# Kernel optimization log

Hardware: AMD Instinct MI355X
Metric: run time of the kernel (lower is better)

The kernel has to match this reference:

```python
import jax, jax.numpy as jnp
import numpy as np

ANCHORS = np.array([[10,13],[16,30],[33,23],[30,61],[62,45],[59,119],[116,90],[156,198],[373,326]], dtype=np.float32)
STRIDES = [32, 16, 8]
MASKS = [[6,7,8],[3,4,5],[0,1,2]]
N_CLASSES = 80
IGNORE_THRESH = 0.7
NUM_A = 3


def _bce_logits(x, z):
    # binary_cross_entropy_with_logits, elementwise (reduction applied by caller)
    return jnp.maximum(x, 0.0) - x * z + jnp.log1p(jnp.exp(-jnp.abs(x)))


def _layer_loss(output, labels, stride, anch_mask):
    B, C, H, W = output.shape
    n_ch = 5 + N_CLASSES
    dtype = output.dtype
    ref_wh = jnp.asarray(ANCHORS / stride, dtype)              # (9,2) all anchors in grid units
    m_anch = ref_wh[jnp.asarray(anch_mask)]                    # (3,2) anchors for this layer
    group = anch_mask[0] // 3                                   # which triple of ref anchors matches this layer

    # (B, A, H, W, n_ch) raw logits
    out = output.reshape(B, NUM_A, n_ch, H, W).transpose(0, 1, 3, 4, 2)

    # decoded pred boxes (cx, cy, w, h) in grid units
    xs = jnp.arange(W, dtype=dtype)
    ys = jnp.arange(H, dtype=dtype)
    px = jax.nn.sigmoid(out[..., 0]) + xs[None, None, None, :]
    py = jax.nn.sigmoid(out[..., 1]) + ys[None, None, :, None]
    pw = jnp.exp(out[..., 2]) * m_anch[:, 0][None, :, None, None]
    ph = jnp.exp(out[..., 3]) * m_anch[:, 1][None, :, None, None]
    pred = jnp.stack([px, py, pw, ph], axis=-1)                # (B,A,H,W,4)

    NC = NUM_A * H * W

    def build_one(pred_b, lab):
        # lab: (nL, 5) = [class, x, y, w, h] normalized; all rows assumed valid
        tx = lab[:, 1] * W; ty = lab[:, 2] * H
        tw = lab[:, 3] * W; th = lab[:, 4] * H
        ti = tx.astype(jnp.int32); tj = ty.astype(jnp.int32)
        wh = jnp.stack([tw, th], axis=-1)                      # (nL,2)

        # anchor IoU (boxes anchored at origin) against all 9 ref anchors
        mn = jnp.minimum(wh[:, None, :], ref_wh[None, :, :])
        en = jnp.prod((mn > 0).astype(dtype), axis=-1)
        inter = jnp.prod(mn, axis=-1) * en
        a_iou = inter / (jnp.prod(wh, -1)[:, None] + jnp.prod(ref_wh, -1)[None, :] - inter)
        best_all = jnp.argmax(a_iou, axis=1)                   # (nL,)
        best_n = best_all % 3
        matched = (best_all // 3) == group                     # truth belongs to this layer

        # pairwise IoU pred boxes vs truth boxes (cxcywh)
        tb = jnp.stack([tx, ty, tw, th], axis=-1)              # (nL,4)
        pf = pred_b.reshape(-1, 4)                             # (AHW,4)
        tl = jnp.maximum(pf[:, None, :2] - pf[:, None, 2:] / 2, tb[None, :, :2] - tb[None, :, 2:] / 2)
        br = jnp.minimum(pf[:, None, :2] + pf[:, None, 2:] / 2, tb[None, :, :2] + tb[None, :, 2:] / 2)
        en2 = jnp.prod((tl < br).astype(dtype), axis=-1)
        inter2 = jnp.prod(br - tl, axis=-1) * en2
        pious = inter2 / (jnp.prod(pf[:, 2:], -1)[:, None] + jnp.prod(tb[:, 2:], -1)[None, :] - inter2)
        obj = (jnp.max(pious, axis=1) <= IGNORE_THRESH).astype(dtype)  # (AHW,) = ~ignore

        # scatter matched truths into (a, j, i) cells; unmatched go to dummy slot NC
        lin = jnp.where(matched, (best_n * H + tj) * W + ti, NC)
        obj = jnp.concatenate([obj, jnp.zeros((1,), dtype)]).at[lin].set(1.0)[:NC].reshape(NUM_A, H, W)
        sel = jnp.zeros((NC + 1,), dtype).at[lin].set(1.0)[:NC].reshape(NUM_A, H, W)
        sval = jnp.sqrt(2.0 - tw * th / (H * W))
        scale = jnp.zeros((NC + 1,), dtype).at[lin].set(sval)[:NC].reshape(NUM_A, H, W)

        cls = lab[:, 0].astype(jnp.int32)
        rows = jnp.concatenate([
            (tx - ti.astype(dtype))[:, None],
            (ty - tj.astype(dtype))[:, None],
            jnp.log(tw / m_anch[best_n, 0] + 1e-16)[:, None],
            jnp.log(th / m_anch[best_n, 1] + 1e-16)[:, None],
            jnp.ones((lab.shape[0], 1), dtype),
            jax.nn.one_hot(cls, N_CLASSES, dtype=dtype)], axis=-1)      # (nL, n_ch)
        target = jnp.zeros((NC + 1, n_ch), dtype).at[lin].set(rows)[:NC].reshape(NUM_A, H, W, n_ch)
        return target, obj, sel, scale

    target, obj, sel, scale = jax.vmap(build_one)(pred, labels)

    sel_e = sel[..., None]
    sc_e = scale[..., None]
    oxy = out[..., :2] * sel_e;              txy = target[..., :2] * sel_e
    owh = out[..., 2:4] * sel_e * sc_e;      twh = target[..., 2:4] * sel_e * sc_e
    o4 = out[..., 4] * obj;                  t4 = target[..., 4] * obj
    ocl = out[..., 5:] * sel_e;              tcl = target[..., 5:] * sel_e

    loss_xy = jnp.sum(_bce_logits(oxy, txy) * sc_e * sc_e)
    loss_wh = jnp.sum((owh - twh) ** 2) / 2
    loss_obj = jnp.sum(_bce_logits(o4, t4))
    loss_cls = jnp.sum(_bce_logits(ocl, tcl))
    return loss_xy + loss_wh + loss_obj + loss_cls


def setup_inputs() -> dict:
    key = jax.random.key(0)
    k0, k1, k2, kc, kxy, kwh = jax.random.split(key, 6)
    B, nL = 16, 50
    output0 = jax.random.normal(k0, (B, 255, 19, 19), dtype=jnp.float32)
    output1 = jax.random.normal(k1, (B, 255, 38, 38), dtype=jnp.float32)
    output2 = jax.random.normal(k2, (B, 255, 76, 76), dtype=jnp.float32)
    cls = jax.random.randint(kc, (B, nL, 1), 0, N_CLASSES).astype(jnp.float32)
    xy = jax.random.uniform(kxy, (B, nL, 2), minval=0.05, maxval=0.95)
    wh = jax.random.uniform(kwh, (B, nL, 2), minval=0.05, maxval=0.4)
    targets = jnp.concatenate([cls, xy, wh], axis=-1)  # [class, x, y, w, h], all rows valid
    return {"output0": output0, "output1": output1, "output2": output2, "targets": targets}


def reference(output0, output1, output2, targets):
    outs = [output0, output1, output2]
    loss = jnp.float32(0.0)
    for layer_no, o in enumerate(outs):
        loss = loss + _layer_loss(o, targets, STRIDES[layer_no], MASKS[layer_no])
    return loss
```

## Files before the change

kernel.cpp:

```cpp
#include <hip/hip_runtime.h>
#include <math.h>

#define N_LABELS 50
#define NCLS 80
#define LOG2C 0.693147180559945f
#define N_CORR_BLOCKS 12
#define N_MAIN_BLOCKS 736
#define N_BLOCKS (N_MAIN_BLOCKS + N_CORR_BLOCKS)

__device__ __constant__ float d_anchors[9][2] = {
    {10.f,13.f},{16.f,30.f},{33.f,23.f},{30.f,61.f},{62.f,45.f},
    {59.f,119.f},{116.f,90.f},{156.f,198.f},{373.f,326.f}
};

__device__ float g_slots[64];
__device__ int   g_count;

__device__ __forceinline__ float softplus_f(float x) {
    return fmaxf(x, 0.f) + __logf(1.f + __expf(-fabsf(x)));
}
__device__ __forceinline__ float bce_f(float x, float z) {
    return fmaxf(x, 0.f) - x * z + __logf(1.f + __expf(-fabsf(x)));
}
__device__ __forceinline__ float sigmoid_f(float x) {
    return __builtin_amdgcn_rcpf(1.f + __expf(-x));
}

template<int H, int W, int GROUP>
__device__ __forceinline__ float main_part(const float* __restrict__ out,
        const float* __restrict__ tgt, int b, int chunk,
        float4* sbox, float* sta)
{
    constexpr int HW = H * W;
    constexpr int NC = 3 * HW;
    constexpr int STRIDE = 608 / W;
    int tid = threadIdx.x;

    if (tid < N_LABELS) {
        const float* lp = tgt + ((size_t)b * N_LABELS + tid) * 5;
        float tx = lp[1] * (float)W, ty = lp[2] * (float)H;
        float tw = lp[3] * (float)W, th = lp[4] * (float)H;
        sbox[tid] = make_float4(tx - 0.5f*tw, ty - 0.5f*th, tx + 0.5f*tw, ty + 0.5f*th);
        sta[tid] = tw * th * (0.7f / 1.7f);
    }
    __syncthreads();

    const float* ob = out + (size_t)b * 255 * HW;
    int c0i = chunk * 512 + tid;
    float x0[2], x1[2], y0[2], y1[2], p07[2], c4v[2], whb[2];
    bool valid[2], ign[2];

    #pragma unroll
    for (int k = 0; k < 2; ++k) {
        int cell = c0i + k * 256;
        valid[k] = (cell < NC);
        int cc = valid[k] ? cell : 0;
        int a = cc / HW, rem = cc - a * HW;
        int hh = rem / W, ww = rem - hh * W;
        const float* base = ob + (size_t)a * 85 * HW + rem;
        float c0 = base[0];
        float c1 = base[HW];
        float c2 = base[2 * (size_t)HW];
        float c3 = base[3 * (size_t)HW];
        c4v[k] = base[4 * (size_t)HW];
        float aw = d_anchors[GROUP*3 + a][0] * (1.f / (float)STRIDE);
        float ah = d_anchors[GROUP*3 + a][1] * (1.f / (float)STRIDE);
        float pw = __expf(c2) * aw, ph = __expf(c3) * ah;
        float px = sigmoid_f(c0) + (float)ww;
        float py = sigmoid_f(c1) + (float)hh;
        x0[k] = px - 0.5f*pw; x1[k] = px + 0.5f*pw;
        y0[k] = py - 0.5f*ph; y1[k] = py + 0.5f*ph;
        p07[k] = pw * ph * (0.7f / 1.7f);
        whb[k] = 0.5f * (c2*c2 + c3*c3);
        ign[k] = false;
    }

    #pragma unroll 5
    for (int l = 0; l < N_LABELS; ++l) {
        float4 tb = sbox[l];
        float ta07 = sta[l];
        #pragma unroll
        for (int k = 0; k < 2; ++k) {
            float w_ = fminf(x1[k], tb.z) - fmaxf(x0[k], tb.x);
            float h_ = fminf(y1[k], tb.w) - fmaxf(y0[k], tb.y);
            bool hit = (fminf(w_, h_) > 0.f) && (w_ * h_ > ta07 + p07[k]);
            ign[k] = ign[k] || hit;
        }
    }

    float lsum = 0.f;
    #pragma unroll
    for (int k = 0; k < 2; ++k)
        if (valid[k])
            lsum += (ign[k] ? LOG2C : softplus_f(c4v[k])) + 80.f * LOG2C + whb[k];
    return lsum;
}

template<int H, int W, int STRIDE, int GROUP>
__device__ __forceinline__ float corr_part(const float* __restrict__ out,
        const float* __restrict__ tgt, int bbase,
        float4 (*sbox)[N_LABELS], int* slin)
{
    constexpr int HW = H * W;
    int tid = threadIdx.x, wid = tid >> 6, lane = tid & 63;
    int b = bbase + wid;

    float tx=0, ty=0, tw=0, th=0, lw=0, lh=0, sc=0;
    int lin = -1, cls = 0;
    if (lane < N_LABELS) {
        const float* lp = tgt + ((size_t)b * N_LABELS + lane) * 5;
        cls = (int)lp[0];
        tx = lp[1] * (float)W; ty = lp[2] * (float)H;
        tw = lp[3] * (float)W; th = lp[4] * (float)H;
        float ta = tw * th;
        sbox[wid][lane] = make_float4(tx - 0.5f*tw, ty - 0.5f*th, tx + 0.5f*tw, ty + 0.5f*th);
        float best_iou = -1.f; int best = 0;
        #pragma unroll
        for (int kk = 0; kk < 9; ++kk) {
            float rw = d_anchors[kk][0] * (1.f / (float)STRIDE);
            float rh = d_anchors[kk][1] * (1.f / (float)STRIDE);
            float mx = fminf(tw, rw), my = fminf(th, rh);
            float inter = (mx > 0.f && my > 0.f) ? mx * my : 0.f;
            float iou = inter / (ta + rw * rh - inter);
            if (iou > best_iou) { best_iou = iou; best = kk; }
        }
        int bn = best - (best / 3) * 3;
        float aw = d_anchors[GROUP*3 + bn][0] * (1.f / (float)STRIDE);
        float ah = d_anchors[GROUP*3 + bn][1] * (1.f / (float)STRIDE);
        lw = __logf(tw / aw + 1e-16f);
        lh = __logf(th / ah + 1e-16f);
        sc = sqrtf(2.f - tw * th * (1.f / (float)HW));
        if (best / 3 == GROUP) {
            int ti = (int)tx, tj = (int)ty;
            lin = (bn * H + tj) * W + ti;
        }
    }
    slin[wid * 64 + lane] = lin;
    __syncthreads();

    bool active = (lin >= 0);
    if (active) {
        for (int l2 = lane + 1; l2 < N_LABELS; ++l2)
            if (slin[wid * 64 + l2] == lin) active = false;
    }

    float lsum = 0.f;
    if (active) {
        int a = lin / HW, rem = lin - a * HW;
        int hh = rem / W, ww = rem - hh * W;
        const float* base = out + ((size_t)b * 255 + (size_t)a * 85) * HW + rem;
        float c0 = base[0];
        float c1 = base[HW];
        float c2 = base[2 * (size_t)HW];
        float c3 = base[3 * (size_t)HW];
        float c4 = base[4 * (size_t)HW];
        float aw = d_anchors[GROUP*3 + a][0] * (1.f / (float)STRIDE);
        float ah = d_anchors[GROUP*3 + a][1] * (1.f / (float)STRIDE);
        float pw = __expf(c2) * aw, ph = __expf(c3) * ah;
        float px = sigmoid_f(c0) + (float)ww;
        float py = sigmoid_f(c1) + (float)hh;
        float X0 = px - 0.5f*pw, X1 = px + 0.5f*pw;
        float Y0 = py - 0.5f*ph, Y1 = py + 0.5f*ph;
        float p07 = pw * ph * (0.7f / 1.7f);
        bool ign = false;
        for (int l = 0; l < N_LABELS; ++l) {
            float4 tb = sbox[wid][l];
            float ta07 = (tb.z - tb.x) * (tb.w - tb.y) * (0.7f / 1.7f);
            float w_ = fminf(X1, tb.z) - fmaxf(X0, tb.x);
            float h_ = fminf(Y1, tb.w) - fmaxf(Y0, tb.y);
            ign = ign || ((fminf(w_, h_) > 0.f) && (w_ * h_ > ta07 + p07));
        }
        float baseobj = ign ? LOG2C : softplus_f(c4);
        lsum += bce_f(c4, 1.f) - baseobj;
        float s2 = sc * sc;
        float txf = tx - (float)(int)tx, tyf = ty - (float)(int)ty;
        lsum += (bce_f(c0, txf) + bce_f(c1, tyf)) * s2;
        float dw = c2 - lw, dh = c3 - lh;
        lsum += 0.5f * (dw*dw + dh*dh) * s2;
        float csum = 0.f;
        for (int c = 0; c < NCLS; ++c) {
            float lg = base[(size_t)(5 + c) * HW];
            csum += bce_f(lg, (c == cls) ? 1.f : 0.f);
        }
        lsum += csum - 80.f * LOG2C;
    }
    return lsum;
}

__global__ __launch_bounds__(256) void yolo_main(
        const float* __restrict__ o0, const float* __restrict__ o1,
        const float* __restrict__ o2, const float* __restrict__ tgt,
        float* __restrict__ loss)
{
    __shared__ float4 sbox[4][N_LABELS];
    __shared__ float  sta4[4][N_LABELS];
    __shared__ int    slin[4 * 64];
    __shared__ float  wsums[4];
    __shared__ int    sflag;
    int bid = blockIdx.x, tid = threadIdx.x;

    float lsum;
    if (bid < N_CORR_BLOCKS) {
        int layer = bid >> 2, bbase = (bid & 3) * 4;
        if (layer == 0)      lsum = corr_part<19,19,32,2>(o0, tgt, bbase, sbox, slin);
        else if (layer == 1) lsum = corr_part<38,38,16,1>(o1, tgt, bbase, sbox, slin);
        else                 lsum = corr_part<76,76,8,0>(o2, tgt, bbase, sbox, slin);
    } else {
        int mb = bid - N_CORR_BLOCKS;
        if (mb < 48) {
            lsum = main_part<19,19,2>(o0, tgt, mb / 3, mb % 3, &sbox[0][0], &sta4[0][0]);
        } else if (mb < 192) {
            int id = mb - 48;
            lsum = main_part<38,38,1>(o1, tgt, id / 9, id % 9, &sbox[0][0], &sta4[0][0]);
        } else {
            int id = mb - 192;
            lsum = main_part<76,76,0>(o2, tgt, id / 34, id % 34, &sbox[0][0], &sta4[0][0]);
        }
    }

    #pragma unroll
    for (int off = 32; off > 0; off >>= 1)
        lsum += __shfl_down(lsum, off);
    if ((tid & 63) == 0) wsums[tid >> 6] = lsum;
    __syncthreads();

    if (tid == 0) {
        float tot = wsums[0] + wsums[1] + wsums[2] + wsums[3];
        float old = atomicAdd(&g_slots[bid & 63], tot);
        asm volatile("" :: "v"(old) : "memory");
        int cnt = atomicAdd(&g_count, 1);
        sflag = (cnt == N_BLOCKS - 1) ? 1 : 0;
    }
    __syncthreads();

    if (sflag && tid < 64) {
        float v = __hip_atomic_load(&g_slots[tid], __ATOMIC_RELAXED, __HIP_MEMORY_SCOPE_AGENT);
        #pragma unroll
        for (int off = 32; off > 0; off >>= 1)
            v += __shfl_down(v, off);
        __hip_atomic_store(&g_slots[tid], 0.f, __ATOMIC_RELAXED, __HIP_MEMORY_SCOPE_AGENT);
        if (tid == 0) {
            *loss = v;
            __hip_atomic_store(&g_count, 0, __ATOMIC_RELAXED, __HIP_MEMORY_SCOPE_AGENT);
        }
    }
}

extern "C" void kernel_launch(void* const* d_in, const int* in_sizes, int n_in,
                              void* d_out, int out_size, void* d_ws, size_t ws_size,
                              hipStream_t stream) {
    const float* o0  = (const float*)d_in[0];
    const float* o1  = (const float*)d_in[1];
    const float* o2  = (const float*)d_in[2];
    const float* tgt = (const float*)d_in[3];
    float* loss = (float*)d_out;
    yolo_main<<<N_BLOCKS, 256, 0, stream>>>(o0, o1, o2, tgt, loss);
}
```

Measured before the change: 27.77 us.

## Spread completion counters across padded slots and branchless ignore test

Replaces the single global completion counter with 64 per-slot counters padded to separate cache lines, plus a second-level done counter, so the 748 blocks no longer all contend on one atomic. Each slot's last arriver bumps the done counter, and the final one reduces the slots. Separately, the IoU ignore test is rewritten as a running max of a min-combined margin using fma, avoiding boolean logic in the inner label loop. This adds a two-level atomic protocol, and the ignore decision may differ slightly at boundary cases because of the fma rounding.

```diff
diff --git a/kernel.cpp b/kernel.cpp
--- a/kernel.cpp
+++ b/kernel.cpp
@@ -13,8 +13,9 @@
     {59.f,119.f},{116.f,90.f},{156.f,198.f},{373.f,326.f}
 };
 
-__device__ float g_slots[64];
-__device__ int   g_count;
+__device__ float g_slots[64 * 32];
+__device__ int   g_scnt[64 * 32];
+__device__ int   g_done;
 
 __device__ __forceinline__ float softplus_f(float x) {
     return fmaxf(x, 0.f) + __logf(1.f + __expf(-fabsf(x)));
@@ -47,8 +48,8 @@
 
     const float* ob = out + (size_t)b * 255 * HW;
     int c0i = chunk * 512 + tid;
-    float x0[2], x1[2], y0[2], y1[2], p07[2], c4v[2], whb[2];
-    bool valid[2], ign[2];
+    float x0[2], x1[2], y0[2], y1[2], p07[2], c4v[2], whb[2], viol[2];
+    bool valid[2];
 
     #pragma unroll
     for (int k = 0; k < 2; ++k) {
@@ -72,7 +73,7 @@
         y0[k] = py - 0.5f*ph; y1[k] = py + 0.5f*ph;
         p07[k] = pw * ph * (0.7f / 1.7f);
         whb[k] = 0.5f * (c2*c2 + c3*c3);
-        ign[k] = false;
+        viol[k] = -1.f;
     }
 
     #pragma unroll 5
@@ -83,8 +84,9 @@
         for (int k = 0; k < 2; ++k) {
             float w_ = fminf(x1[k], tb.z) - fmaxf(x0[k], tb.x);
             float h_ = fminf(y1[k], tb.w) - fmaxf(y0[k], tb.y);
-            bool hit = (fminf(w_, h_) > 0.f) && (w_ * h_ > ta07 + p07[k]);
-            ign[k] = ign[k] || hit;
+            float t  = ta07 + p07[k];
+            float m = fminf(fminf(w_, h_), __builtin_fmaf(w_, h_, -t));
+            viol[k] = fmaxf(viol[k], m);
         }
     }
 
@@ -92,7 +94,7 @@
     #pragma unroll
     for (int k = 0; k < 2; ++k)
         if (valid[k])
-            lsum += (ign[k] ? LOG2C : softplus_f(c4v[k])) + 80.f * LOG2C + whb[k];
+            lsum += ((viol[k] > 0.f) ? LOG2C : softplus_f(c4v[k])) + 80.f * LOG2C + whb[k];
     return lsum;
 }
 
@@ -226,22 +228,31 @@
 
     if (tid == 0) {
         float tot = wsums[0] + wsums[1] + wsums[2] + wsums[3];
-        float old = atomicAdd(&g_slots[bid & 63], tot);
+        int s = bid & 63;
+        int expect = (s < 44) ? 12 : 11;
+        float old = atomicAdd(&g_slots[s * 32], tot);
         asm volatile("" :: "v"(old) : "memory");
-        int cnt = atomicAdd(&g_count, 1);
-        sflag = (cnt == N_BLOCKS - 1) ? 1 : 0;
+        int c = atomicAdd(&g_scnt[s * 32], 1);
+        int flag = 0;
+        if (c == expect - 1) {
+            asm volatile("" :: "v"(c) : "memory");
+            int d = atomicAdd(&g_done, 1);
+            flag = (d == 63) ? 1 : 0;
+        }
+        sflag = flag;
     }
     __syncthreads();
 
     if (sflag && tid < 64) {
-        float v = __hip_atomic_load(&g_slots[tid], __ATOMIC_RELAXED, __HIP_MEMORY_SCOPE_AGENT);
+        float v = __hip_atomic_load(&g_slots[tid * 32], __ATOMIC_RELAXED, __HIP_MEMORY_SCOPE_AGENT);
         #pragma unroll
         for (int off = 32; off > 0; off >>= 1)
             v += __shfl_down(v, off);
-        __hip_atomic_store(&g_slots[tid], 0.f, __ATOMIC_RELAXED, __HIP_MEMORY_SCOPE_AGENT);
+        __hip_atomic_store(&g_slots[tid * 32], 0.f, __ATOMIC_RELAXED, __HIP_MEMORY_SCOPE_AGENT);
+        __hip_atomic_store(&g_scnt[tid * 32], 0, __ATOMIC_RELAXED, __HIP_MEMORY_SCOPE_AGENT);
         if (tid == 0) {
             *loss = v;
-            __hip_atomic_store(&g_count, 0, __ATOMIC_RELAXED, __HIP_MEMORY_SCOPE_AGENT);
+            __hip_atomic_store(&g_done, 0, __ATOMIC_RELAXED, __HIP_MEMORY_SCOPE_AGENT);
         }
     }
 }
```

New measurement: 24.03 us. 13.4% less time.
